# Kernel tuning notes

Measured on AMD Instinct MI355X. Metric: run time of the kernel, lower is better.

## Reference

```python
import jax, jax.numpy as jnp
import numpy as np

L = 3
EPSILON = 0.01
T = 1.0
L1_EPS = 1e-12  # torch F.normalize default eps


def _cdist(x, y):
    # Euclidean pairwise distance, (b, n, d) x (b, m, d) -> (b, n, m)
    x2 = jnp.sum(x * x, axis=-1, keepdims=True)            # (b, n, 1)
    y2 = jnp.sum(y * y, axis=-1)[:, None, :]               # (b, 1, m)
    xy = jnp.einsum('bnd,bmd->bnm', x, y)                  # (b, n, m)
    return jnp.sqrt(jnp.maximum(x2 + y2 - 2.0 * xy, 0.0))


def setup_inputs() -> dict:
    key = jax.random.key(0)
    k1, k2 = jax.random.split(key)
    B, S, D = 4, 2048, 512
    A = jax.random.uniform(k1, (B, S, S), dtype=jnp.float32)
    V = jax.random.normal(k2, (B, S, D), dtype=jnp.float32)
    return {"A": A, "V": V}


def reference(A, V):
    M = jnp.matmul(A, V)  # (b, s, d)
    for _ in range(L):
        Md = jax.lax.stop_gradient(M)
        Vd = jax.lax.stop_gradient(V)
        dist = _cdist(Md, Vd)                               # (b, s, s)
        w = 1.0 / (dist + EPSILON)                          # norm == 'L2'
        ww = w * A                                          # (b, s, s)
        l1 = jnp.maximum(jnp.sum(jnp.abs(ww), axis=-1, keepdims=True), L1_EPS)
        ww_norm = ww / l1
        M = (1.0 - T) * M + T * jnp.matmul(ww_norm, V)
    return M
```

## Files before the change

kernel.cpp:

```cpp
#include <hip/hip_runtime.h>


typedef __bf16 bf16;
typedef bf16 bf16x4 __attribute__((ext_vector_type(4)));
typedef bf16 bf16x8 __attribute__((ext_vector_type(8)));
typedef float f32x4 __attribute__((ext_vector_type(4)));

#define S_DIM 2048
#define D_DIM 512
#define NB    4
#define EPSILON 0.01f

#define AS1 __attribute__((address_space(1)))
#define AS3 __attribute__((address_space(3)))

__global__ void cast_kernel(const float* __restrict__ in, bf16* __restrict__ out,
                            int n4, float* __restrict__ m2z) {
  if (blockIdx.x < 32) m2z[blockIdx.x * 256 + threadIdx.x] = 0.f;
  int i = blockIdx.x * blockDim.x + threadIdx.x;
  if (i >= n4) return;
  float4 v = ((const float4*)in)[i];
  bf16x4 o = { (bf16)v.x, (bf16)v.y, (bf16)v.z, (bf16)v.w };
  ((bf16x4*)out)[i] = o;
}

__global__ void vprep_kernel(const float* __restrict__ V, bf16* __restrict__ Vbf,
                             bf16* __restrict__ Vt, float* __restrict__ v2) {
  __shared__ float tile[64][68];
  int b  = blockIdx.y;
  int r0 = blockIdx.x * 64;
  const float* Vb = V   + (size_t)b * S_DIM * D_DIM;
  bf16*       Vfb = Vbf + (size_t)b * S_DIM * D_DIM;
  bf16*       Vtb = Vt  + (size_t)b * S_DIM * D_DIM;
  float*      v2b = v2  + (size_t)b * S_DIM;
  int tx = threadIdx.x & 15, ty = threadIdx.x >> 4;
  float acc2[4] = { 0.f, 0.f, 0.f, 0.f };
  for (int c = 0; c < 8; ++c) {
    int c0 = c * 64;
#pragma unroll
    for (int i = 0; i < 4; ++i) {
      int r = ty + i * 16;
      float4 v = *(const float4*)(Vb + (size_t)(r0 + r) * D_DIM + (c0 + tx * 4));
      tile[r][tx * 4 + 0] = v.x; tile[r][tx * 4 + 1] = v.y;
      tile[r][tx * 4 + 2] = v.z; tile[r][tx * 4 + 3] = v.w;
      bf16x4 o = { (bf16)v.x, (bf16)v.y, (bf16)v.z, (bf16)v.w };
      *(bf16x4*)(Vfb + (size_t)(r0 + r) * D_DIM + (c0 + tx * 4)) = o;
#pragma unroll
      for (int j = 0; j < 4; ++j) { float f = (float)o[j]; acc2[i] += f * f; }
    }
    __syncthreads();
#pragma unroll
    for (int i = 0; i < 4; ++i) {
      int cc = ty + i * 16;
      bf16x4 o = { (bf16)tile[tx * 4 + 0][cc], (bf16)tile[tx * 4 + 1][cc],
                   (bf16)tile[tx * 4 + 2][cc], (bf16)tile[tx * 4 + 3][cc] };
      *(bf16x4*)(Vtb + (size_t)(c0 + cc) * S_DIM + (r0 + tx * 4)) = o;
    }
    __syncthreads();
  }
#pragma unroll
  for (int i = 0; i < 4; ++i) {
    float s = acc2[i];
    s += __shfl_xor(s, 1); s += __shfl_xor(s, 2);
    s += __shfl_xor(s, 4); s += __shfl_xor(s, 8);
    if (tx == 0) v2b[r0 + ty + i * 16] = s;
  }
}

__global__ __launch_bounds__(256, 4)
void gemmP_kernel(const bf16* __restrict__ Amat, const bf16* __restrict__ Bmat,
                  int M, int N, int K,
                  const float* __restrict__ m2, const float* __restrict__ v2,
                  const bf16* __restrict__ Aw, bf16* __restrict__ Wout,
                  float* __restrict__ l1p, float* __restrict__ m2z) {
  const int bz = blockIdx.z;
  const int gx  = gridDim.x;
  const int nwg = gx * gridDim.y;
  int lin = blockIdx.y * gx + blockIdx.x;
  lin = (lin & 7) * (nwg >> 3) + (lin >> 3);
  const int bx = lin % gx;
  const int by = lin / gx;

  if (bx == 0 && threadIdx.x < 128)
    m2z[(size_t)bz * S_DIM + by * 128 + threadIdx.x] = 0.f;

  const int row0 = by * 128;
  const int col0 = bx * 128;
  const bf16* Ab = Amat + (size_t)bz * M * K;
  const bf16* Bb = Bmat + (size_t)bz * N * K;

  __shared__ char smem[33792];
  bf16*  ldsA = (bf16*)smem;
  bf16*  ldsB = (bf16*)(smem + 16384);
  float* ldsW = (float*)smem;

  const int tid  = threadIdx.x;
  const int wave = tid >> 6;
  const int lane = tid & 63;
  const int wr   = wave >> 1;
  const int wc   = wave & 1;
  const int q    = lane >> 4;
  const int c16  = lane & 15;
  const int srow = lane >> 3;
  const int scol = ((lane & 7) ^ srow) * 8;

  f32x4 acc[4][4] = {};

  for (int k0 = 0; k0 < K; k0 += 64) {
#pragma unroll
    for (int i = 0; i < 4; ++i) {
      int slot = wave * 4 + i;
      int r = slot * 8 + srow;
      __builtin_amdgcn_global_load_lds(
          (const AS1 void*)(Ab + (size_t)(row0 + r) * K + (k0 + scol)),
          (AS3 void*)(ldsA + slot * 512), 16, 0, 0);
      __builtin_amdgcn_global_load_lds(
          (const AS1 void*)(Bb + (size_t)(col0 + r) * K + (k0 + scol)),
          (AS3 void*)(ldsB + slot * 512), 16, 0, 0);
    }
    __syncthreads();

#pragma unroll
    for (int kk = 0; kk < 2; ++kk) {
      bf16x8 afr[4], bfr[4];
#pragma unroll
      for (int mt = 0; mt < 4; ++mt) {
        int R = wr * 64 + mt * 16 + c16;
        int p = ((kk << 2) + q) ^ (c16 & 7);
        afr[mt] = *(const bf16x8*)(ldsA + (size_t)R * 64 + p * 8);
      }
#pragma unroll
      for (int nt = 0; nt < 4; ++nt) {
        int R = wc * 64 + nt * 16 + c16;
        int p = ((kk << 2) + q) ^ (c16 & 7);
        bfr[nt] = *(const bf16x8*)(ldsB + (size_t)R * 64 + p * 8);
      }
#pragma unroll
      for (int mt = 0; mt < 4; ++mt)
#pragma unroll
        for (int nt = 0; nt < 4; ++nt)
          acc[mt][nt] = __builtin_amdgcn_mfma_f32_16x16x32_bf16(afr[mt], bfr[nt], acc[mt][nt], 0, 0, 0);
    }
    __syncthreads();
  }

  const int rowBase = row0 + wr * 64 + q * 4;
  const int colBase = col0 + wc * 64 + c16;

  {
    const float* m2b = m2 + (size_t)bz * M;
    const float* v2b = v2 + (size_t)bz * N;
    float v2v[4];
#pragma unroll
    for (int nt = 0; nt < 4; ++nt) v2v[nt] = v2b[colBase + nt * 16];
#pragma unroll
    for (int mt = 0; mt < 4; ++mt)
#pragma unroll
      for (int r = 0; r < 4; ++r) {
        float m2v = m2b[rowBase + mt * 16 + r];
#pragma unroll
        for (int nt = 0; nt < 4; ++nt) {
          float d2 = fmaxf(m2v + v2v[nt] - 2.f * acc[mt][nt][r], 0.f);
          acc[mt][nt][r] = __builtin_amdgcn_rcpf(__builtin_amdgcn_sqrtf(d2) + EPSILON);
        }
      }
  }

  const int lr  = tid >> 3;
  const int sub = tid & 7;
#pragma unroll
  for (int h = 0; h < 2; ++h) {
    __syncthreads();
    if (wr == h) {
#pragma unroll
      for (int mt = 0; mt < 4; ++mt)
#pragma unroll
        for (int nt = 0; nt < 4; ++nt)
#pragma unroll
          for (int r = 0; r < 4; ++r)
            ldsW[(mt * 16 + q * 4 + r) * 132 + wc * 64 + nt * 16 + c16] = acc[mt][nt][r];
    }
    __syncthreads();
#pragma unroll
    for (int h2 = 0; h2 < 2; ++h2) {
      int rloc = lr + 32 * h2;
      int gi = row0 + 64 * h + rloc;
      const float* wp = ldsW + rloc * 132 + sub * 16;
      float4 w0 = *(const float4*)(wp + 0);
      float4 w1 = *(const float4*)(wp + 4);
      float4 w2 = *(const float4*)(wp + 8);
      float4 w3 = *(const float4*)(wp + 12);
      float wv_[16] = { w0.x, w0.y, w0.z, w0.w, w1.x, w1.y, w1.z, w1.w,
                        w2.x, w2.y, w2.z, w2.w, w3.x, w3.y, w3.z, w3.w };
      const bf16* ap = Aw + (size_t)bz * M * N + (size_t)gi * N + (col0 + sub * 16);
      bf16x8 a0 = *(const bf16x8*)(ap);
      bf16x8 a1 = *(const bf16x8*)(ap + 8);
      bf16x8 o0, o1;
      float rs = 0.f;
#pragma unroll
      for (int e = 0; e < 8; ++e) {
        float x0 = wv_[e] * (float)a0[e];
        float x1 = wv_[e + 8] * (float)a1[e];
        o0[e] = (bf16)x0; o1[e] = (bf16)x1;
        rs += fabsf(x0) + fabsf(x1);
      }
      bf16* op = Wout + (size_t)bz * M * N + (size_t)gi * N + (col0 + sub * 16);
      *(bf16x8*)(op)     = o0;
      *(bf16x8*)(op + 8) = o1;
      rs += __shfl_xor(rs, 1);
      rs += __shfl_xor(rs, 2);
      rs += __shfl_xor(rs, 4);
      if (sub == 0) l1p[((size_t)bx * NB + bz) * M + gi] = rs;
    }
  }
}

template <int SCALED>
__global__ __launch_bounds__(256, 4)
void gemmwv_kernel(const bf16* __restrict__ Amat, const bf16* __restrict__ Bmat,
                   const float* __restrict__ l1p, bf16* __restrict__ Mo,
                   float* __restrict__ Fo, float* __restrict__ m2out) {
  const int bz = blockIdx.z;
  const int gx  = gridDim.x;
  const int nwg = gx * gridDim.y;
  int lin = blockIdx.y * gx + blockIdx.x;
  lin = (lin & 7) * (nwg >> 3) + (lin >> 3);
  const int bx = lin % gx;
  const int by = lin / gx;

  const int row0 = by * 128;
  const int col0 = bx * 64;
  const bf16* Ab = Amat + (size_t)bz * S_DIM * S_DIM;
  const bf16* Bb = Bmat + (size_t)bz * S_DIM * D_DIM;

  __shared__ char smem[24576];
  bf16*  ldsA = (bf16*)smem;
  bf16*  ldsB = (bf16*)(smem + 16384);
  float* ldsW = (float*)smem;

  const int tid  = threadIdx.x;
  const int wave = tid >> 6;
  const int lane = tid & 63;
  const int wr   = wave >> 1;
  const int wc   = wave & 1;
  const int q    = lane >> 4;
  const int c16  = lane & 15;
  const int srow = lane >> 3;
  const int scol = ((lane & 7) ^ srow) * 8;

  f32x4 acc[4][2] = {};

  for (int k0 = 0; k0 < S_DIM; k0 += 64) {
#pragma unroll
    for (int i = 0; i < 4; ++i) {
      int slot = wave * 4 + i;
      int r = slot * 8 + srow;
      __builtin_amdgcn_global_load_lds(
          (const AS1 void*)(Ab + (size_t)(row0 + r) * S_DIM + (k0 + scol)),
          (AS3 void*)(ldsA + slot * 512), 16, 0, 0);
    }
#pragma unroll
    for (int i = 0; i < 2; ++i) {
      int slot = wave * 2 + i;
      int r = slot * 8 + srow;
      __builtin_amdgcn_global_load_lds(
          (const AS1 void*)(Bb + (size_t)(col0 + r) * S_DIM + (k0 + scol)),
          (AS3 void*)(ldsB + slot * 512), 16, 0, 0);
    }
    __syncthreads();

#pragma unroll
    for (int kk = 0; kk < 2; ++kk) {
      bf16x8 afr[4], bfr[2];
      const int p = ((kk << 2) + q) ^ (c16 & 7);
#pragma unroll
      for (int mt = 0; mt < 4; ++mt)
        afr[mt] = *(const bf16x8*)(ldsA + (size_t)(wr * 64 + mt * 16 + c16) * 64 + p * 8);
#pragma unroll
      for (int nt = 0; nt < 2; ++nt)
        bfr[nt] = *(const bf16x8*)(ldsB + (size_t)(wc * 32 + nt * 16 + c16) * 64 + p * 8);
#pragma unroll
      for (int mt = 0; mt < 4; ++mt)
#pragma unroll
        for (int nt = 0; nt < 2; ++nt)
          acc[mt][nt] = __builtin_amdgcn_mfma_f32_16x16x32_bf16(afr[mt], bfr[nt], acc[mt][nt], 0, 0, 0);
    }
    __syncthreads();
  }

  const int lr  = tid >> 2;
  const int sub = tid & 3;
#pragma unroll
  for (int h = 0; h < 2; ++h) {
    __syncthreads();
    if (wr == h) {
#pragma unroll
      for (int mt = 0; mt < 4; ++mt)
#pragma unroll
        for (int nt = 0; nt < 2; ++nt)
#pragma unroll
          for (int r = 0; r < 4; ++r)
            ldsW[(mt * 16 + q * 4 + r) * 68 + wc * 32 + nt * 16 + c16] = acc[mt][nt][r];
    }
    __syncthreads();
    const int gi = row0 + 64 * h + lr;
    const float* wp = ldsW + lr * 68 + sub * 16;
    float4 w0 = *(const float4*)(wp + 0);
    float4 w1 = *(const float4*)(wp + 4);
    float4 w2 = *(const float4*)(wp + 8);
    float4 w3 = *(const float4*)(wp + 12);
    float wv_[16] = { w0.x, w0.y, w0.z, w0.w, w1.x, w1.y, w1.z, w1.w,
                      w2.x, w2.y, w2.z, w2.w, w3.x, w3.y, w3.z, w3.w };
    float sc = 1.f;
    if (SCALED >= 1) {
      float l1v = 0.f;
#pragma unroll
      for (int e = 0; e < 16; ++e) l1v += l1p[((size_t)e * NB + bz) * S_DIM + gi];
      sc = __builtin_amdgcn_rcpf(fmaxf(l1v, 1e-12f));
    }
#pragma unroll
    for (int e = 0; e < 16; ++e) wv_[e] *= sc;
    if (SCALED == 2) {
      float* op = Fo + (size_t)bz * S_DIM * D_DIM + (size_t)gi * D_DIM + col0 + sub * 16;
      float4 o0 = { wv_[0], wv_[1], wv_[2], wv_[3] };
      float4 o1 = { wv_[4], wv_[5], wv_[6], wv_[7] };
      float4 o2 = { wv_[8], wv_[9], wv_[10], wv_[11] };
      float4 o3 = { wv_[12], wv_[13], wv_[14], wv_[15] };
      *(float4*)(op + 0)  = o0; *(float4*)(op + 4)  = o1;
      *(float4*)(op + 8)  = o2; *(float4*)(op + 12) = o3;
    } else {
      bf16x8 o0, o1;
      float s = 0.f;
#pragma unroll
      for (int e = 0; e < 8; ++e) {
        o0[e] = (bf16)wv_[e];     s += wv_[e] * wv_[e];
        o1[e] = (bf16)wv_[e + 8]; s += wv_[e + 8] * wv_[e + 8];
      }
      bf16* op = Mo + (size_t)bz * S_DIM * D_DIM + (size_t)gi * D_DIM + col0 + sub * 16;
      *(bf16x8*)(op)     = o0;
      *(bf16x8*)(op + 8) = o1;
      s += __shfl_xor(s, 1);
      s += __shfl_xor(s, 2);
      if (sub == 0) atomicAdd(m2out + (size_t)bz * S_DIM + gi, s);
    }
  }
}

extern "C" void kernel_launch(void* const* d_in, const int* in_sizes, int n_in,
                              void* d_out, int out_size, void* d_ws, size_t ws_size,
                              hipStream_t stream) {
  const float* A = (const float*)d_in[0];
  const float* V = (const float*)d_in[1];
  float* out = (float*)d_out;

  char* ws = (char*)d_ws;
  bf16* Abf = (bf16*)ws;   ws += (size_t)NB * S_DIM * S_DIM * 2;
  bf16* Vbf = (bf16*)ws;   ws += (size_t)NB * S_DIM * D_DIM * 2;
  bf16* Vt  = (bf16*)ws;   ws += (size_t)NB * S_DIM * D_DIM * 2;
  bf16* Mbf = (bf16*)ws;   ws += (size_t)NB * S_DIM * D_DIM * 2;
  bf16* Wbf = (bf16*)ws;   ws += (size_t)NB * S_DIM * S_DIM * 2;
  float* v2 = (float*)ws;  ws += (size_t)NB * S_DIM * 4;
  float* m2a = (float*)ws; ws += (size_t)NB * S_DIM * 4;
  float* m2b = (float*)ws; ws += (size_t)NB * S_DIM * 4;
  float* l1p = (float*)ws; ws += (size_t)16 * NB * S_DIM * 4;

  int nA4 = NB * S_DIM * S_DIM / 4;
  cast_kernel<<<nA4 / 256, 256, 0, stream>>>(A, Abf, nA4, m2a);
  vprep_kernel<<<dim3(S_DIM / 64, NB), 256, 0, stream>>>(V, Vbf, Vt, v2);

  gemmwv_kernel<0><<<dim3(D_DIM / 64, S_DIM / 128, NB), 256, 0, stream>>>(
      Abf, Vt, nullptr, Mbf, nullptr, m2a);

  gemmP_kernel<<<dim3(16, 16, NB), 256, 0, stream>>>(
      Mbf, Vbf, S_DIM, S_DIM, D_DIM, m2a, v2, Abf, Wbf, l1p, m2b);
  gemmwv_kernel<1><<<dim3(D_DIM / 64, S_DIM / 128, NB), 256, 0, stream>>>(
      Wbf, Vt, l1p, Mbf, nullptr, m2b);

  gemmP_kernel<<<dim3(16, 16, NB), 256, 0, stream>>>(
      Mbf, Vbf, S_DIM, S_DIM, D_DIM, m2b, v2, Abf, Wbf, l1p, m2a);
  gemmwv_kernel<1><<<dim3(D_DIM / 64, S_DIM / 128, NB), 256, 0, stream>>>(
      Wbf, Vt, l1p, Mbf, nullptr, m2a);

  gemmP_kernel<<<dim3(16, 16, NB), 256, 0, stream>>>(
      Mbf, Vbf, S_DIM, S_DIM, D_DIM, m2a, v2, Abf, Wbf, l1p, m2b);
  gemmwv_kernel<2><<<dim3(D_DIM / 64, S_DIM / 128, NB), 256, 0, stream>>>(
      Wbf, Vt, l1p, nullptr, out, nullptr);
}
```

Before: 328.2 us.

## Split-K the WV GEMM into two bf16 partials, folding reduction and scaling into the next stage

```diff
diff --git a/kernel.cpp b/kernel.cpp
--- a/kernel.cpp
+++ b/kernel.cpp
@@ -14,9 +14,7 @@
 #define AS1 __attribute__((address_space(1)))
 #define AS3 __attribute__((address_space(3)))
 
-__global__ void cast_kernel(const float* __restrict__ in, bf16* __restrict__ out,
-                            int n4, float* __restrict__ m2z) {
-  if (blockIdx.x < 32) m2z[blockIdx.x * 256 + threadIdx.x] = 0.f;
+__global__ void cast_kernel(const float* __restrict__ in, bf16* __restrict__ out, int n4) {
   int i = blockIdx.x * blockDim.x + threadIdx.x;
   if (i >= n4) return;
   float4 v = ((const float4*)in)[i];
@@ -67,12 +65,12 @@
   }
 }
 
+template <int SCALED>
 __global__ __launch_bounds__(256, 4)
-void gemmP_kernel(const bf16* __restrict__ Amat, const bf16* __restrict__ Bmat,
-                  int M, int N, int K,
-                  const float* __restrict__ m2, const float* __restrict__ v2,
+void gemmP_kernel(const bf16* __restrict__ Pin, const bf16* __restrict__ Bmat,
+                  const float* __restrict__ v2, const float* __restrict__ l1in,
                   const bf16* __restrict__ Aw, bf16* __restrict__ Wout,
-                  float* __restrict__ l1p, float* __restrict__ m2z) {
+                  float* __restrict__ l1out) {
   const int bz = blockIdx.z;
   const int gx  = gridDim.x;
   const int nwg = gx * gridDim.y;
@@ -81,18 +79,17 @@
   const int bx = lin % gx;
   const int by = lin / gx;
 
-  if (bx == 0 && threadIdx.x < 128)
-    m2z[(size_t)bz * S_DIM + by * 128 + threadIdx.x] = 0.f;
-
   const int row0 = by * 128;
   const int col0 = bx * 128;
-  const bf16* Ab = Amat + (size_t)bz * M * K;
-  const bf16* Bb = Bmat + (size_t)bz * N * K;
-
-  __shared__ char smem[33792];
-  bf16*  ldsA = (bf16*)smem;
-  bf16*  ldsB = (bf16*)(smem + 16384);
-  float* ldsW = (float*)smem;
+  const bf16* p0base = Pin + (size_t)bz * S_DIM * D_DIM;
+  const bf16* p1base = p0base + (size_t)NB * S_DIM * D_DIM;
+  const bf16* Bb = Bmat + (size_t)bz * S_DIM * D_DIM;
+
+  __shared__ char smem[34304];
+  bf16*  ldsA  = (bf16*)smem;
+  bf16*  ldsB  = (bf16*)(smem + 16384);
+  float* ldsW  = (float*)smem;
+  float* m2lds = (float*)(smem + 33792);
 
   const int tid  = threadIdx.x;
   const int wave = tid >> 6;
@@ -104,18 +101,41 @@
   const int srow = lane >> 3;
   const int scol = ((lane & 7) ^ srow) * 8;
 
+  float sc[4];
+#pragma unroll
+  for (int i = 0; i < 4; ++i) {
+    if (SCALED) {
+      const int row = row0 + (wave * 4 + i) * 8 + srow;
+      float s = 0.f;
+#pragma unroll
+      for (int e = 0; e < 16; ++e) s += l1in[((size_t)e * NB + bz) * S_DIM + row];
+      sc[i] = __builtin_amdgcn_rcpf(fmaxf(s, 1e-12f));
+    } else {
+      sc[i] = 1.f;
+    }
+  }
+
   f32x4 acc[4][4] = {};
-
-  for (int k0 = 0; k0 < K; k0 += 64) {
+  float m2a[4] = { 0.f, 0.f, 0.f, 0.f };
+
+  for (int k0 = 0; k0 < D_DIM; k0 += 64) {
 #pragma unroll
     for (int i = 0; i < 4; ++i) {
-      int slot = wave * 4 + i;
-      int r = slot * 8 + srow;
+      const int slot = wave * 4 + i;
+      const int r = slot * 8 + srow;
+      const size_t off = (size_t)(row0 + r) * D_DIM + (k0 + scol);
+      bf16x8 a0 = *(const bf16x8*)(p0base + off);
+      bf16x8 a1 = *(const bf16x8*)(p1base + off);
+      bf16x8 o;
+#pragma unroll
+      for (int e = 0; e < 8; ++e) {
+        float v = ((float)a0[e] + (float)a1[e]) * sc[i];
+        m2a[i] += v * v;
+        o[e] = (bf16)v;
+      }
+      *(bf16x8*)(ldsA + slot * 512 + lane * 8) = o;
       __builtin_amdgcn_global_load_lds(
-          (const AS1 void*)(Ab + (size_t)(row0 + r) * K + (k0 + scol)),
-          (AS3 void*)(ldsA + slot * 512), 16, 0, 0);
-      __builtin_amdgcn_global_load_lds(
-          (const AS1 void*)(Bb + (size_t)(col0 + r) * K + (k0 + scol)),
+          (const AS1 void*)(Bb + (size_t)(col0 + r) * D_DIM + (k0 + scol)),
           (AS3 void*)(ldsB + slot * 512), 16, 0, 0);
     }
     __syncthreads();
@@ -144,12 +164,18 @@
     __syncthreads();
   }
 
-  const int rowBase = row0 + wr * 64 + q * 4;
+#pragma unroll
+  for (int i = 0; i < 4; ++i) {
+    float s = m2a[i];
+    s += __shfl_xor(s, 1); s += __shfl_xor(s, 2); s += __shfl_xor(s, 4);
+    if ((lane & 7) == 0) m2lds[(wave * 4 + i) * 8 + srow] = s;
+  }
+  __syncthreads();
+
   const int colBase = col0 + wc * 64 + c16;
 
   {
-    const float* m2b = m2 + (size_t)bz * M;
-    const float* v2b = v2 + (size_t)bz * N;
+    const float* v2b = v2 + (size_t)bz * S_DIM;
     float v2v[4];
 #pragma unroll
     for (int nt = 0; nt < 4; ++nt) v2v[nt] = v2b[colBase + nt * 16];
@@ -157,7 +183,7 @@
     for (int mt = 0; mt < 4; ++mt)
 #pragma unroll
       for (int r = 0; r < 4; ++r) {
-        float m2v = m2b[rowBase + mt * 16 + r];
+        float m2v = m2lds[wr * 64 + mt * 16 + q * 4 + r];
 #pragma unroll
         for (int nt = 0; nt < 4; ++nt) {
           float d2 = fmaxf(m2v + v2v[nt] - 2.f * acc[mt][nt][r], 0.f);
@@ -192,7 +218,7 @@
       float4 w3 = *(const float4*)(wp + 12);
       float wv_[16] = { w0.x, w0.y, w0.z, w0.w, w1.x, w1.y, w1.z, w1.w,
                         w2.x, w2.y, w2.z, w2.w, w3.x, w3.y, w3.z, w3.w };
-      const bf16* ap = Aw + (size_t)bz * M * N + (size_t)gi * N + (col0 + sub * 16);
+      const bf16* ap = Aw + (size_t)bz * S_DIM * S_DIM + (size_t)gi * S_DIM + (col0 + sub * 16);
       bf16x8 a0 = *(const bf16x8*)(ap);
       bf16x8 a1 = *(const bf16x8*)(ap + 8);
       bf16x8 o0, o1;
@@ -204,23 +230,24 @@
         o0[e] = (bf16)x0; o1[e] = (bf16)x1;
         rs += fabsf(x0) + fabsf(x1);
       }
-      bf16* op = Wout + (size_t)bz * M * N + (size_t)gi * N + (col0 + sub * 16);
+      bf16* op = Wout + (size_t)bz * S_DIM * S_DIM + (size_t)gi * S_DIM + (col0 + sub * 16);
       *(bf16x8*)(op)     = o0;
       *(bf16x8*)(op + 8) = o1;
       rs += __shfl_xor(rs, 1);
       rs += __shfl_xor(rs, 2);
       rs += __shfl_xor(rs, 4);
-      if (sub == 0) l1p[((size_t)bx * NB + bz) * M + gi] = rs;
-    }
-  }
-}
-
-template <int SCALED>
+      if (sub == 0) l1out[((size_t)bx * NB + bz) * S_DIM + gi] = rs;
+    }
+  }
+}
+
 __global__ __launch_bounds__(256, 4)
-void gemmwv_kernel(const bf16* __restrict__ Amat, const bf16* __restrict__ Bmat,
-                   const float* __restrict__ l1p, bf16* __restrict__ Mo,
-                   float* __restrict__ Fo, float* __restrict__ m2out) {
-  const int bz = blockIdx.z;
+void gemm_kernel(const bf16* __restrict__ Amat, const bf16* __restrict__ Bmat,
+                 int M, int N, int K, bf16* __restrict__ Cp) {
+  const int bz = blockIdx.z >> 1;
+  const int ks = blockIdx.z & 1;
+  const int kbeg = ks * (K >> 1), kend = kbeg + (K >> 1);
+
   const int gx  = gridDim.x;
   const int nwg = gx * gridDim.y;
   int lin = blockIdx.y * gx + blockIdx.x;
@@ -229,11 +256,11 @@
   const int by = lin / gx;
 
   const int row0 = by * 128;
-  const int col0 = bx * 64;
-  const bf16* Ab = Amat + (size_t)bz * S_DIM * S_DIM;
-  const bf16* Bb = Bmat + (size_t)bz * S_DIM * D_DIM;
-
-  __shared__ char smem[24576];
+  const int col0 = bx * 128;
+  const bf16* Ab = Amat + (size_t)bz * M * K;
+  const bf16* Bb = Bmat + (size_t)bz * N * K;
+
+  __shared__ char smem[33792];
   bf16*  ldsA = (bf16*)smem;
   bf16*  ldsB = (bf16*)(smem + 16384);
   float* ldsW = (float*)smem;
@@ -248,102 +275,103 @@
   const int srow = lane >> 3;
   const int scol = ((lane & 7) ^ srow) * 8;
 
-  f32x4 acc[4][2] = {};
-
-  for (int k0 = 0; k0 < S_DIM; k0 += 64) {
+  f32x4 acc[4][4] = {};
+
+  for (int k0 = kbeg; k0 < kend; k0 += 64) {
 #pragma unroll
     for (int i = 0; i < 4; ++i) {
       int slot = wave * 4 + i;
       int r = slot * 8 + srow;
       __builtin_amdgcn_global_load_lds(
-          (const AS1 void*)(Ab + (size_t)(row0 + r) * S_DIM + (k0 + scol)),
+          (const AS1 void*)(Ab + (size_t)(row0 + r) * K + (k0 + scol)),
           (AS3 void*)(ldsA + slot * 512), 16, 0, 0);
-    }
-#pragma unroll
-    for (int i = 0; i < 2; ++i) {
-      int slot = wave * 2 + i;
-      int r = slot * 8 + srow;
       __builtin_amdgcn_global_load_lds(
-          (const AS1 void*)(Bb + (size_t)(col0 + r) * S_DIM + (k0 + scol)),
+          (const AS1 void*)(Bb + (size_t)(col0 + r) * K + (k0 + scol)),
           (AS3 void*)(ldsB + slot * 512), 16, 0, 0);
     }
     __syncthreads();
 
 #pragma unroll
     for (int kk = 0; kk < 2; ++kk) {
-      bf16x8 afr[4], bfr[2];
-      const int p = ((kk << 2) + q) ^ (c16 & 7);
+      bf16x8 afr[4], bfr[4];
+#pragma unroll
+      for (int mt = 0; mt < 4; ++mt) {
+        int R = wr * 64 + mt * 16 + c16;
+        int p = ((kk << 2) + q) ^ (c16 & 7);
+        afr[mt] = *(const bf16x8*)(ldsA + (size_t)R * 64 + p * 8);
+      }
+#pragma unroll
+      for (int nt = 0; nt < 4; ++nt) {
+        int R = wc * 64 + nt * 16 + c16;
+        int p = ((kk << 2) + q) ^ (c16 & 7);
+        bfr[nt] = *(const bf16x8*)(ldsB + (size_t)R * 64 + p * 8);
+      }
 #pragma unroll
       for (int mt = 0; mt < 4; ++mt)
-        afr[mt] = *(const bf16x8*)(ldsA + (size_t)(wr * 64 + mt * 16 + c16) * 64 + p * 8);
-#pragma unroll
-      for (int nt = 0; nt < 2; ++nt)
-        bfr[nt] = *(const bf16x8*)(ldsB + (size_t)(wc * 32 + nt * 16 + c16) * 64 + p * 8);
+#pragma unroll
+        for (int nt = 0; nt < 4; ++nt)
+          acc[mt][nt] = __builtin_amdgcn_mfma_f32_16x16x32_bf16(afr[mt], bfr[nt], acc[mt][nt], 0, 0, 0);
+    }
+    __syncthreads();
+  }
+
+  const int lr  = tid >> 3;
+  const int sub = tid & 7;
+#pragma unroll
+  for (int h = 0; h < 2; ++h) {
+    __syncthreads();
+    if (wr == h) {
 #pragma unroll
       for (int mt = 0; mt < 4; ++mt)
 #pragma unroll
-        for (int nt = 0; nt < 2; ++nt)
-          acc[mt][nt] = __builtin_amdgcn_mfma_f32_16x16x32_bf16(afr[mt], bfr[nt], acc[mt][nt], 0, 0, 0);
-    }
-    __syncthreads();
-  }
-
-  const int lr  = tid >> 2;
-  const int sub = tid & 3;
-#pragma unroll
-  for (int h = 0; h < 2; ++h) {
-    __syncthreads();
-    if (wr == h) {
-#pragma unroll
-      for (int mt = 0; mt < 4; ++mt)
-#pragma unroll
-        for (int nt = 0; nt < 2; ++nt)
+        for (int nt = 0; nt < 4; ++nt)
 #pragma unroll
           for (int r = 0; r < 4; ++r)
-            ldsW[(mt * 16 + q * 4 + r) * 68 + wc * 32 + nt * 16 + c16] = acc[mt][nt][r];
-    }
-    __syncthreads();
-    const int gi = row0 + 64 * h + lr;
-    const float* wp = ldsW + lr * 68 + sub * 16;
-    float4 w0 = *(const float4*)(wp + 0);
-    float4 w1 = *(const float4*)(wp + 4);
-    float4 w2 = *(const float4*)(wp + 8);
-    float4 w3 = *(const float4*)(wp + 12);
-    float wv_[16] = { w0.x, w0.y, w0.z, w0.w, w1.x, w1.y, w1.z, w1.w,
-                      w2.x, w2.y, w2.z, w2.w, w3.x, w3.y, w3.z, w3.w };
-    float sc = 1.f;
-    if (SCALED >= 1) {
-      float l1v = 0.f;
-#pragma unroll
-      for (int e = 0; e < 16; ++e) l1v += l1p[((size_t)e * NB + bz) * S_DIM + gi];
-      sc = __builtin_amdgcn_rcpf(fmaxf(l1v, 1e-12f));
-    }
-#pragma unroll
-    for (int e = 0; e < 16; ++e) wv_[e] *= sc;
-    if (SCALED == 2) {
-      float* op = Fo + (size_t)bz * S_DIM * D_DIM + (size_t)gi * D_DIM + col0 + sub * 16;
-      float4 o0 = { wv_[0], wv_[1], wv_[2], wv_[3] };
-      float4 o1 = { wv_[4], wv_[5], wv_[6], wv_[7] };
-      float4 o2 = { wv_[8], wv_[9], wv_[10], wv_[11] };
-      float4 o3 = { wv_[12], wv_[13], wv_[14], wv_[15] };
-      *(float4*)(op + 0)  = o0; *(float4*)(op + 4)  = o1;
-      *(float4*)(op + 8)  = o2; *(float4*)(op + 12) = o3;
-    } else {
+            ldsW[(mt * 16 + q * 4 + r) * 132 + wc * 64 + nt * 16 + c16] = acc[mt][nt][r];
+    }
+    __syncthreads();
+#pragma unroll
+    for (int h2 = 0; h2 < 2; ++h2) {
+      int rloc = lr + 32 * h2;
+      int gi = row0 + 64 * h + rloc;
+      const float* wp = ldsW + rloc * 132 + sub * 16;
+      float4 w0 = *(const float4*)(wp + 0);
+      float4 w1 = *(const float4*)(wp + 4);
+      float4 w2 = *(const float4*)(wp + 8);
+      float4 w3 = *(const float4*)(wp + 12);
+      float wv_[16] = { w0.x, w0.y, w0.z, w0.w, w1.x, w1.y, w1.z, w1.w,
+                        w2.x, w2.y, w2.z, w2.w, w3.x, w3.y, w3.z, w3.w };
+      bf16* Cb = Cp + ((size_t)ks * NB + bz) * ((size_t)M * N);
       bf16x8 o0, o1;
-      float s = 0.f;
-#pragma unroll
-      for (int e = 0; e < 8; ++e) {
-        o0[e] = (bf16)wv_[e];     s += wv_[e] * wv_[e];
-        o1[e] = (bf16)wv_[e + 8]; s += wv_[e + 8] * wv_[e + 8];
-      }
-      bf16* op = Mo + (size_t)bz * S_DIM * D_DIM + (size_t)gi * D_DIM + col0 + sub * 16;
+#pragma unroll
+      for (int e = 0; e < 8; ++e) { o0[e] = (bf16)wv_[e]; o1[e] = (bf16)wv_[e + 8]; }
+      bf16* op = Cb + (size_t)gi * N + (col0 + sub * 16);
       *(bf16x8*)(op)     = o0;
       *(bf16x8*)(op + 8) = o1;
-      s += __shfl_xor(s, 1);
-      s += __shfl_xor(s, 2);
-      if (sub == 0) atomicAdd(m2out + (size_t)bz * S_DIM + gi, s);
-    }
-  }
+    }
+  }
+}
+
+__global__ void reduce_kernel(const bf16* __restrict__ part, const float* __restrict__ l1p,
+                              float* __restrict__ Fo) {
+  int wave = threadIdx.x >> 6, lane = threadIdx.x & 63;
+  int rg = blockIdx.x * 4 + wave;
+  const bf16* p0 = part + (size_t)rg * D_DIM + lane * 8;
+  const bf16* p1 = p0 + (size_t)NB * S_DIM * D_DIM;
+  bf16x8 a = *(const bf16x8*)p0;
+  bf16x8 b = *(const bf16x8*)p1;
+  float v[8];
+#pragma unroll
+  for (int e = 0; e < 8; ++e) v[e] = (float)a[e] + (float)b[e];
+  int bb = rg >> 11, row = rg & (S_DIM - 1);
+  float l1v = 0.f;
+#pragma unroll
+  for (int e = 0; e < 16; ++e) l1v += l1p[((size_t)e * NB + bb) * S_DIM + row];
+  float sc = __builtin_amdgcn_rcpf(fmaxf(l1v, 1e-12f));
+  float4 o0 = { v[0] * sc, v[1] * sc, v[2] * sc, v[3] * sc };
+  float4 o1 = { v[4] * sc, v[5] * sc, v[6] * sc, v[7] * sc };
+  float* op = Fo + (size_t)rg * D_DIM + lane * 8;
+  *(float4*)(op) = o0; *(float4*)(op + 4) = o1;
 }
 
 extern "C" void kernel_launch(void* const* d_in, const int* in_sizes, int n_in,
@@ -357,32 +385,33 @@
   bf16* Abf = (bf16*)ws;   ws += (size_t)NB * S_DIM * S_DIM * 2;
   bf16* Vbf = (bf16*)ws;   ws += (size_t)NB * S_DIM * D_DIM * 2;
   bf16* Vt  = (bf16*)ws;   ws += (size_t)NB * S_DIM * D_DIM * 2;
-  bf16* Mbf = (bf16*)ws;   ws += (size_t)NB * S_DIM * D_DIM * 2;
   bf16* Wbf = (bf16*)ws;   ws += (size_t)NB * S_DIM * S_DIM * 2;
-  float* v2 = (float*)ws;  ws += (size_t)NB * S_DIM * 4;
-  float* m2a = (float*)ws; ws += (size_t)NB * S_DIM * 4;
-  float* m2b = (float*)ws; ws += (size_t)NB * S_DIM * 4;
-  float* l1p = (float*)ws; ws += (size_t)16 * NB * S_DIM * 4;
+  bf16* part = (bf16*)ws;  ws += (size_t)2 * NB * S_DIM * D_DIM * 2;
+  float* v2  = (float*)ws;  ws += (size_t)NB * S_DIM * 4;
+  float* l1pA = (float*)ws; ws += (size_t)16 * NB * S_DIM * 4;
+  float* l1pB = (float*)ws; ws += (size_t)16 * NB * S_DIM * 4;
 
   int nA4 = NB * S_DIM * S_DIM / 4;
-  cast_kernel<<<nA4 / 256, 256, 0, stream>>>(A, Abf, nA4, m2a);
+  cast_kernel<<<nA4 / 256, 256, 0, stream>>>(A, Abf, nA4);
   vprep_kernel<<<dim3(S_DIM / 64, NB), 256, 0, stream>>>(V, Vbf, Vt, v2);
 
-  gemmwv_kernel<0><<<dim3(D_DIM / 64, S_DIM / 128, NB), 256, 0, stream>>>(
-      Abf, Vt, nullptr, Mbf, nullptr, m2a);
-
-  gemmP_kernel<<<dim3(16, 16, NB), 256, 0, stream>>>(
-      Mbf, Vbf, S_DIM, S_DIM, D_DIM, m2a, v2, Abf, Wbf, l1p, m2b);
-  gemmwv_kernel<1><<<dim3(D_DIM / 64, S_DIM / 128, NB), 256, 0, stream>>>(
-      Wbf, Vt, l1p, Mbf, nullptr, m2b);
-
-  gemmP_kernel<<<dim3(16, 16, NB), 256, 0, stream>>>(
-      Mbf, Vbf, S_DIM, S_DIM, D_DIM, m2b, v2, Abf, Wbf, l1p, m2a);
-  gemmwv_kernel<1><<<dim3(D_DIM / 64, S_DIM / 128, NB), 256, 0, stream>>>(
-      Wbf, Vt, l1p, Mbf, nullptr, m2a);
-
-  gemmP_kernel<<<dim3(16, 16, NB), 256, 0, stream>>>(
-      Mbf, Vbf, S_DIM, S_DIM, D_DIM, m2a, v2, Abf, Wbf, l1p, m2b);
-  gemmwv_kernel<2><<<dim3(D_DIM / 64, S_DIM / 128, NB), 256, 0, stream>>>(
-      Wbf, Vt, l1p, nullptr, out, nullptr);
-}
+  gemm_kernel<<<dim3(D_DIM / 128, S_DIM / 128, NB * 2), 256, 0, stream>>>(
+      Abf, Vt, S_DIM, D_DIM, S_DIM, part);
+
+  gemmP_kernel<0><<<dim3(16, 16, NB), 256, 0, stream>>>(
+      part, Vbf, v2, nullptr, Abf, Wbf, l1pA);
+  gemm_kernel<<<dim3(D_DIM / 128, S_DIM / 128, NB * 2), 256, 0, stream>>>(
+      Wbf, Vt, S_DIM, D_DIM, S_DIM, part);
+
+  gemmP_kernel<1><<<dim3(16, 16, NB), 256, 0, stream>>>(
+      part, Vbf, v2, l1pA, Abf, Wbf, l1pB);
+  gemm_kernel<<<dim3(D_DIM / 128, S_DIM / 128, NB * 2), 256, 0, stream>>>(
+      Wbf, Vt, S_DIM, D_DIM, S_DIM, part);
+
+  gemmP_kernel<1><<<dim3(16, 16, NB), 256, 0, stream>>>(
+      part, Vbf, v2, l1pB, Abf, Wbf, l1pA);
+  gemm_kernel<<<dim3(D_DIM / 128, S_DIM / 128, NB * 2), 256, 0, stream>>>(
+      Wbf, Vt, S_DIM, D_DIM, S_DIM, part);
+
+  reduce_kernel<<<NB * S_DIM / 4, 256, 0, stream>>>(part, l1pA, out);
+}
```

Measured after the change: 389.1 us. 1.19x slower.
